# Kernel optimization log

Hardware: AMD Instinct MI355X
Metric: run time of the kernel (lower is better)

The kernel has to match this reference:

```python
import jax, jax.numpy as jnp
import numpy as np

N_NODES = 8192
N_EDGES = 524288
IN_DIM = 256
HID1 = 128
HID2 = 64


def setup_inputs() -> dict:
    key = jax.random.key(0)
    ks = jax.random.split(key, 10)
    s = 0.05
    x = jax.random.normal(ks[0], (N_NODES, IN_DIM), dtype=jnp.float32)
    edge_index = jax.random.randint(ks[1], (2, N_EDGES), 0, N_NODES, dtype=jnp.int64)
    W1 = jax.random.normal(ks[2], (IN_DIM, HID1), dtype=jnp.float32) * s
    b1 = jnp.zeros((HID1,), dtype=jnp.float32)
    W2 = jax.random.normal(ks[3], (IN_DIM, HID1), dtype=jnp.float32) * s
    b2 = jnp.zeros((HID1,), dtype=jnp.float32)
    Wmu = jax.random.normal(ks[4], (2 * HID1, HID2), dtype=jnp.float32) * s
    bmu = jnp.zeros((HID2,), dtype=jnp.float32)
    Wlv = jax.random.normal(ks[5], (2 * HID1, HID2), dtype=jnp.float32) * s
    blv = jnp.zeros((HID2,), dtype=jnp.float32)
    return {"x": x, "edge_index": edge_index, "W1": W1, "b1": b1,
            "W2": W2, "b2": b2, "Wmu": Wmu, "bmu": bmu, "Wlv": Wlv, "blv": blv}


def _gcn(x, W, b, row, col, norm, n):
    # linear transform, edge-indexed gather, degree-normalized scale, scatter-add
    h = x @ W                                   # [N, out]
    msg = h[col] * norm[:, None]                # [E+N, out]
    agg = jax.ops.segment_sum(msg, row, num_segments=n)
    return agg + b


def reference(x, edge_index, W1, b1, W2, b2, Wmu, bmu, Wlv, blv):
    n = x.shape[0]
    loop = jnp.arange(n, dtype=edge_index.dtype)
    row = jnp.concatenate([edge_index[0], loop])   # add self-loops (GCNConv default)
    col = jnp.concatenate([edge_index[1], loop])
    deg = jax.ops.segment_sum(jnp.ones_like(row, dtype=x.dtype), row, num_segments=n)
    dinv = jnp.where(deg > 0, jax.lax.rsqrt(deg), 0.0)
    norm = dinv[row] * dinv[col]                   # symmetric D^-1/2 A_hat D^-1/2

    h1 = _gcn(x, W1, b1, row, col, norm, n)
    h2 = _gcn(x, W2, b2, row, col, norm, n)
    hc = jnp.concatenate([h1, h2], axis=1)         # [N, 2*HID1]
    mu = _gcn(hc, Wmu, bmu, row, col, norm, n)
    logvar = _gcn(hc, Wlv, blv, row, col, norm, n)
    z = mu                                         # eval-mode reparametrize -> mu
    adj = jax.nn.sigmoid(z @ z.T)                  # InnerProductDecoder.forward_all
    return adj, mu, logvar
```

## Files before the change

kernel.cpp:

```cpp
#include <hip/hip_runtime.h>
#include <hip/hip_bf16.h>

#define N_NODES 8192
#define N_EDGES 524288
#define TOT_EDGES (N_EDGES + N_NODES)
#define IN_DIM 256
#define HID1 128
#define HID2 64
#define DC 128
#define CAP 192
#define FILL_BLK 520

typedef __attribute__((ext_vector_type(8))) short bf16x8;
typedef __attribute__((ext_vector_type(4))) float f32x4;
typedef __attribute__((ext_vector_type(4))) int   i32x4;
typedef __attribute__((ext_vector_type(4))) unsigned short u16x4;

__device__ __forceinline__ float b2f(unsigned short u){
    unsigned int v = ((unsigned int)u) << 16;
    float f; __builtin_memcpy(&f, &v, 4); return f;
}
__device__ __forceinline__ unsigned short f2b(float f){
    __hip_bfloat16 h = __float2bfloat16(f);
    return *(unsigned short*)&h;
}


__global__ __launch_bounds__(256) void k_pre(const float* __restrict__ W1, const float* __restrict__ W2,
                                             const float* __restrict__ Wmu, const float* __restrict__ Wlv,
                                             const float* __restrict__ b1, const float* __restrict__ b2,
                                             unsigned short* __restrict__ WcT, float* __restrict__ cvec,
                                             float* __restrict__ zbase){
    int b = blockIdx.x, t = threadIdx.x;
    if (b < 8){
        ((f32x4*)zbase)[b*256 + t] = (f32x4){0.f,0.f,0.f,0.f};
    } else {
        int r = (b - 8)*2 + (t >> 7);
        int j = t & 127;
        const float* Wsel = (j < 64) ? Wmu : Wlv;
        int jj = j & 63;
        float acc = 0.f;
        for (int k=0;k<HID1;k++){
            acc += W1[r*HID1+k] * Wsel[k*HID2+jj] + W2[r*HID1+k] * Wsel[(HID1+k)*HID2+jj];
        }
        WcT[(size_t)j*IN_DIM + r] = f2b(acc);
        if (r == 0){
            float c = 0.f;
            for (int k=0;k<HID1;k++){
                c += b1[k]*Wsel[k*HID2+jj] + b2[k]*Wsel[(HID1+k)*HID2+jj];
            }
            cvec[j] = c;
        }
    }
}


__global__ __launch_bounds__(256) void k_fill_gemm(const int* __restrict__ ei, int* __restrict__ fillc,
                                                   unsigned short* __restrict__ slots,
                                                   const float* __restrict__ x,
                                                   const unsigned short* __restrict__ WcT,
                                                   unsigned short* __restrict__ Ubf){
    int b = blockIdx.x, t = threadIdx.x;
    if (b < FILL_BLK){
        int e4 = (b*256 + t)*4;
        if (e4 >= TOT_EDGES) return;
        if (e4 < N_EDGES){
            i32x4 rr = *(const i32x4*)(ei + e4);
            i32x4 cc = *(const i32x4*)(ei + N_EDGES + e4);
            #pragma unroll
            for (int j=0;j<4;j++){
                int s = atomicAdd(&fillc[rr[j]], 1);
                if (s < CAP) slots[(size_t)rr[j]*CAP + s] = (unsigned short)cc[j];
            }
        } else {
            #pragma unroll
            for (int j=0;j<4;j++){
                int r = e4 - N_EDGES + j;
                int s = atomicAdd(&fillc[r], 1);
                if (s < CAP) slots[(size_t)r*CAP + s] = (unsigned short)r;
            }
        }
    } else {
        int l  = t & 63;
        int w  = t >> 6;
        int Ibase = (b - FILL_BLK)*32;
        int Jbase = w*32;
        int lr = l & 15;
        int kg = l >> 4;
        f32x4 acc[2][2];
        #pragma unroll
        for (int mt=0;mt<2;mt++)
            #pragma unroll
            for (int nt=0;nt<2;nt++) acc[mt][nt] = (f32x4){0.f,0.f,0.f,0.f};
        #pragma unroll
        for (int kc=0; kc<IN_DIM/32; kc++){
            bf16x8 a[2], bb[2];
            #pragma unroll
            for (int mt=0;mt<2;mt++){
                const float* xr = x + (size_t)(Ibase+mt*16+lr)*IN_DIM + kc*32 + kg*8;
                f32x4 v0 = *(const f32x4*)xr;
                f32x4 v1 = *(const f32x4*)(xr + 4);
                #pragma unroll
                for (int j=0;j<4;j++){
                    a[mt][j]   = (short)f2b(v0[j]);
                    a[mt][4+j] = (short)f2b(v1[j]);
                }
            }
            #pragma unroll
            for (int nt=0;nt<2;nt++)
                bb[nt] = *(const bf16x8*)(WcT + (size_t)(Jbase+nt*16+lr)*IN_DIM + kc*32 + kg*8);
            #pragma unroll
            for (int mt=0;mt<2;mt++)
                #pragma unroll
                for (int nt=0;nt<2;nt++)
                    acc[mt][nt] = __builtin_amdgcn_mfma_f32_16x16x32_bf16(a[mt], bb[nt], acc[mt][nt], 0, 0, 0);
        }
        #pragma unroll
        for (int mt=0;mt<2;mt++)
            #pragma unroll
            for (int r=0;r<4;r++){
                int grow = Ibase + mt*16 + kg*4 + r;
                #pragma unroll
                for (int nt=0;nt<2;nt++)
                    Ubf[(size_t)grow*DC + Jbase + nt*16 + lr] = f2b(acc[mt][nt][r]);
            }
    }
}


__global__ __launch_bounds__(256) void k_spmm(const unsigned short* __restrict__ IN,
                                              const unsigned short* __restrict__ slots,
                                              const int* __restrict__ fillc,
                                              unsigned short* __restrict__ OUT){
    int tid = threadIdx.x;
    int i = blockIdx.x*4 + (tid >> 6);
    int l  = tid & 15;
    int eg = (tid >> 4) & 3;
    int deg = min(fillc[i], CAP);
    const unsigned short* sl = slots + (size_t)i*CAP;
    float acc[8] = {0.f,0.f,0.f,0.f,0.f,0.f,0.f,0.f};
    for (int e = eg; e < deg; e += 4){
        int c = sl[e];
        float wgt = rsqrtf((float)fillc[c]);
        bf16x8 v = *(const bf16x8*)(IN + (size_t)c*DC + l*8);
        #pragma unroll
        for (int j=0;j<8;j++) acc[j] += wgt * b2f((unsigned short)v[j]);
    }
    #pragma unroll
    for (int j=0;j<8;j++){
        acc[j] += __shfl_xor(acc[j], 16);
        acc[j] += __shfl_xor(acc[j], 32);
    }
    if (eg == 0){
        float di = rsqrtf((float)fillc[i]);
        bf16x8 o;
        #pragma unroll
        for (int j=0;j<8;j++) o[j] = (short)f2b(di*acc[j]);
        *(bf16x8*)(OUT + (size_t)i*DC + l*8) = o;
    }
}


__global__ __launch_bounds__(256) void k_spmm_out(const unsigned short* __restrict__ T,
                                                  const unsigned short* __restrict__ slots,
                                                  const int* __restrict__ fillc,
                                                  const float* __restrict__ cvec,
                                                  const float* __restrict__ bmu, const float* __restrict__ blv,
                                                  float* __restrict__ outMu, float* __restrict__ outLv,
                                                  unsigned short* __restrict__ muBf){
    int tid = threadIdx.x;
    int i = blockIdx.x*4 + (tid >> 6);
    int l  = tid & 15;
    int eg = (tid >> 4) & 3;
    int deg = min(fillc[i], CAP);
    const unsigned short* sl = slots + (size_t)i*CAP;
    float acc[8] = {0.f,0.f,0.f,0.f,0.f,0.f,0.f,0.f};
    float wsum = 0.f;
    for (int e = eg; e < deg; e += 4){
        int c = sl[e];
        float wgt = rsqrtf((float)fillc[c]);
        wsum += wgt;
        bf16x8 v = *(const bf16x8*)(T + (size_t)c*DC + l*8);
        #pragma unroll
        for (int j=0;j<8;j++) acc[j] += wgt * b2f((unsigned short)v[j]);
    }
    #pragma unroll
    for (int j=0;j<8;j++){
        acc[j] += __shfl_xor(acc[j], 16);
        acc[j] += __shfl_xor(acc[j], 32);
    }
    wsum += __shfl_xor(wsum, 16);
    wsum += __shfl_xor(wsum, 32);
    if (eg == 0){
        float di = rsqrtf((float)fillc[i]);
        float sv = di * wsum;
        float val[8];
        #pragma unroll
        for (int j=0;j<8;j++) val[j] = di*acc[j] + sv*cvec[l*8+j];
        if (l < 8){
            f32x4 v0, v1; bf16x8 o;
            #pragma unroll
            for (int j=0;j<8;j++){
                float vv = val[j] + bmu[l*8+j];
                if (j<4) v0[j] = vv; else v1[j-4] = vv;
                o[j] = (short)f2b(vv);
            }
            *(f32x4*)(outMu + (size_t)i*HID2 + l*8)     = v0;
            *(f32x4*)(outMu + (size_t)i*HID2 + l*8 + 4) = v1;
            *(bf16x8*)(muBf + (size_t)i*HID2 + l*8)     = o;
        } else {
            int d = (l-8)*8;
            f32x4 v0, v1;
            #pragma unroll
            for (int j=0;j<8;j++){
                float vv = val[j] + blv[d+j];
                if (j<4) v0[j] = vv; else v1[j-4] = vv;
            }
            *(f32x4*)(outLv + (size_t)i*HID2 + d)     = v0;
            *(f32x4*)(outLv + (size_t)i*HID2 + d + 4) = v1;
        }
    }
}


__global__ __launch_bounds__(256) void k_adj(const unsigned short* __restrict__ mu, float* __restrict__ adj){
    int t  = threadIdx.x;
    int l  = t & 63;
    int w  = t >> 6;
    int wr = w >> 1, wc = w & 1;
    int Ibase = blockIdx.y*128 + wr*64;
    int Jbase = blockIdx.x*128 + wc*64;
    int lr = l & 15;
    int kg = l >> 4;

    bf16x8 afr[4][2], bfr[4][2];
    #pragma unroll
    for (int mt=0; mt<4; mt++){
        const unsigned short* p = mu + (size_t)(Ibase + mt*16 + lr)*HID2 + kg*8;
        afr[mt][0] = *(const bf16x8*)(p);
        afr[mt][1] = *(const bf16x8*)(p + 32);
    }
    #pragma unroll
    for (int nt=0; nt<4; nt++){
        const unsigned short* p = mu + (size_t)(Jbase + nt*16 + lr)*HID2 + kg*8;
        bfr[nt][0] = *(const bf16x8*)(p);
        bfr[nt][1] = *(const bf16x8*)(p + 32);
    }

    f32x4 acc[4][4];
    #pragma unroll
    for (int mt=0; mt<4; mt++)
        #pragma unroll
        for (int nt=0; nt<4; nt++)
            acc[mt][nt] = (f32x4){0.f,0.f,0.f,0.f};

    #pragma unroll
    for (int kc=0; kc<2; kc++)
        #pragma unroll
        for (int mt=0; mt<4; mt++)
            #pragma unroll
            for (int nt=0; nt<4; nt++)
                acc[mt][nt] = __builtin_amdgcn_mfma_f32_16x16x32_bf16(afr[mt][kc], bfr[nt][kc], acc[mt][nt], 0, 0, 0);

    __shared__ float wt[4][16][68];
    float* myt = &wt[w][0][0];
    #pragma unroll
    for (int mt=0; mt<4; mt++){
        asm volatile("s_waitcnt lgkmcnt(0)" ::: "memory");
        #pragma unroll
        for (int nt=0; nt<4; nt++)
            #pragma unroll
            for (int r=0; r<4; r++)
                myt[(kg*4+r)*68 + nt*16 + lr] = acc[mt][nt][r];
        asm volatile("s_waitcnt lgkmcnt(0)" ::: "memory");
        __builtin_amdgcn_sched_barrier(0);
        #pragma unroll
        for (int p=0; p<4; p++){
            int row = p*4 + (l >> 4);
            int col = (l & 15)*4;
            f32x4 v = *(const f32x4*)&myt[row*68 + col];
            f32x4 o;
            #pragma unroll
            for (int j=0;j<4;j++)
                o[j] = __builtin_amdgcn_rcpf(1.f + __expf(-v[j]));
            __builtin_nontemporal_store(o, (f32x4*)(adj + (size_t)(Ibase + mt*16 + row)*N_NODES + Jbase + col));
        }
    }
}


extern "C" void kernel_launch(void* const* d_in, const int* in_sizes, int n_in,
                              void* d_out, int out_size, void* d_ws, size_t ws_size,
                              hipStream_t stream){
    const float* x   = (const float*)d_in[0];
    const int*   ei  = (const int*)  d_in[1];
    const float* W1  = (const float*)d_in[2];
    const float* b1  = (const float*)d_in[3];
    const float* W2  = (const float*)d_in[4];
    const float* b2  = (const float*)d_in[5];
    const float* Wmu = (const float*)d_in[6];
    const float* bmu = (const float*)d_in[7];
    const float* Wlv = (const float*)d_in[8];
    const float* blv = (const float*)d_in[9];

    char* ws = (char*)d_ws;
    int*   fillc  = (int*)  (ws + 0);
    unsigned short* WcT = (unsigned short*)(ws + 32768);
    float* cvec   = (float*)(ws + 98304);
    unsigned short* muBf = (unsigned short*)(ws + 98816);

    float* adj   = (float*)d_out;
    float* outMu = adj + (size_t)N_NODES*N_NODES;
    float* outLv = outMu + (size_t)N_NODES*HID2;

    unsigned short* Ubf   = (unsigned short*)adj;
    unsigned short* Tbf   = (unsigned short*)((char*)adj + 16*1024*1024);
    unsigned short* slots = (unsigned short*)((char*)adj + 32*1024*1024);

    k_pre      <<<136, 256, 0, stream>>>(W1, W2, Wmu, Wlv, b1, b2, WcT, cvec, (float*)ws);
    k_fill_gemm<<<FILL_BLK + 256, 256, 0, stream>>>(ei, fillc, slots, x, WcT, Ubf);
    k_spmm     <<<N_NODES/4, 256, 0, stream>>>(Ubf, slots, fillc, Tbf);
    k_spmm_out <<<N_NODES/4, 256, 0, stream>>>(Tbf, slots, fillc, cvec, bmu, blv,
                                               outMu, outLv, muBf);
    k_adj      <<<dim3(N_NODES/128, N_NODES/128), 256, 0, stream>>>(muBf, adj);
}
```

Baseline: 126.8 us.

## Fold destination norm into first SpMM output so second SpMM skips per-edge weights

The first SpMM now adds the constant bias term and pre-scales each row by its own inverse-sqrt degree, so the second SpMM can sum neighbour rows without weights. This removes the per-edge fillc gather, rsqrt and weight-sum reduction from the second aggregation. The slot writes in the fill kernel become nontemporal stores, and both aggregation loops get unroll-2 hints. Storing the pre-scaled intermediate in bf16 changes rounding slightly.

Result: no change. 126.2 us (-0.4%).

```diff
diff --git a/kernel.cpp b/kernel.cpp
--- a/kernel.cpp
+++ b/kernel.cpp
@@ -70,14 +70,16 @@
             #pragma unroll
             for (int j=0;j<4;j++){
                 int s = atomicAdd(&fillc[rr[j]], 1);
-                if (s < CAP) slots[(size_t)rr[j]*CAP + s] = (unsigned short)cc[j];
+                if (s < CAP) __builtin_nontemporal_store((unsigned short)cc[j],
+                                 slots + (size_t)rr[j]*CAP + s);
             }
         } else {
             #pragma unroll
             for (int j=0;j<4;j++){
                 int r = e4 - N_EDGES + j;
                 int s = atomicAdd(&fillc[r], 1);
-                if (s < CAP) slots[(size_t)r*CAP + s] = (unsigned short)r;
+                if (s < CAP) __builtin_nontemporal_store((unsigned short)r,
+                                 slots + (size_t)r*CAP + s);
             }
         }
     } else {
@@ -131,6 +133,7 @@
 __global__ __launch_bounds__(256) void k_spmm(const unsigned short* __restrict__ IN,
                                               const unsigned short* __restrict__ slots,
                                               const int* __restrict__ fillc,
+                                              const float* __restrict__ cvec,
                                               unsigned short* __restrict__ OUT){
     int tid = threadIdx.x;
     int i = blockIdx.x*4 + (tid >> 6);
@@ -139,6 +142,7 @@
     int deg = min(fillc[i], CAP);
     const unsigned short* sl = slots + (size_t)i*CAP;
     float acc[8] = {0.f,0.f,0.f,0.f,0.f,0.f,0.f,0.f};
+    #pragma unroll 2
     for (int e = eg; e < deg; e += 4){
         int c = sl[e];
         float wgt = rsqrtf((float)fillc[c]);
@@ -155,7 +159,10 @@
         float di = rsqrtf((float)fillc[i]);
         bf16x8 o;
         #pragma unroll
-        for (int j=0;j<8;j++) o[j] = (short)f2b(di*acc[j]);
+        for (int j=0;j<8;j++){
+            float tprime = di*acc[j] + cvec[l*8+j];
+            o[j] = (short)f2b(di*tprime);
+        }
         *(bf16x8*)(OUT + (size_t)i*DC + l*8) = o;
     }
 }
@@ -164,7 +171,6 @@
 __global__ __launch_bounds__(256) void k_spmm_out(const unsigned short* __restrict__ T,
                                                   const unsigned short* __restrict__ slots,
                                                   const int* __restrict__ fillc,
-                                                  const float* __restrict__ cvec,
                                                   const float* __restrict__ bmu, const float* __restrict__ blv,
                                                   float* __restrict__ outMu, float* __restrict__ outLv,
                                                   unsigned short* __restrict__ muBf){
@@ -175,33 +181,25 @@
     int deg = min(fillc[i], CAP);
     const unsigned short* sl = slots + (size_t)i*CAP;
     float acc[8] = {0.f,0.f,0.f,0.f,0.f,0.f,0.f,0.f};
-    float wsum = 0.f;
+    #pragma unroll 2
     for (int e = eg; e < deg; e += 4){
         int c = sl[e];
-        float wgt = rsqrtf((float)fillc[c]);
-        wsum += wgt;
         bf16x8 v = *(const bf16x8*)(T + (size_t)c*DC + l*8);
         #pragma unroll
-        for (int j=0;j<8;j++) acc[j] += wgt * b2f((unsigned short)v[j]);
+        for (int j=0;j<8;j++) acc[j] += b2f((unsigned short)v[j]);
     }
     #pragma unroll
     for (int j=0;j<8;j++){
         acc[j] += __shfl_xor(acc[j], 16);
         acc[j] += __shfl_xor(acc[j], 32);
     }
-    wsum += __shfl_xor(wsum, 16);
-    wsum += __shfl_xor(wsum, 32);
     if (eg == 0){
         float di = rsqrtf((float)fillc[i]);
-        float sv = di * wsum;
-        float val[8];
-        #pragma unroll
-        for (int j=0;j<8;j++) val[j] = di*acc[j] + sv*cvec[l*8+j];
         if (l < 8){
             f32x4 v0, v1; bf16x8 o;
             #pragma unroll
             for (int j=0;j<8;j++){
-                float vv = val[j] + bmu[l*8+j];
+                float vv = di*acc[j] + bmu[l*8+j];
                 if (j<4) v0[j] = vv; else v1[j-4] = vv;
                 o[j] = (short)f2b(vv);
             }
@@ -213,7 +211,7 @@
             f32x4 v0, v1;
             #pragma unroll
             for (int j=0;j<8;j++){
-                float vv = val[j] + blv[d+j];
+                float vv = di*acc[j] + blv[d+j];
                 if (j<4) v0[j] = vv; else v1[j-4] = vv;
             }
             *(f32x4*)(outLv + (size_t)i*HID2 + d)     = v0;
@@ -319,8 +317,8 @@
 
     k_pre      <<<136, 256, 0, stream>>>(W1, W2, Wmu, Wlv, b1, b2, WcT, cvec, (float*)ws);
     k_fill_gemm<<<FILL_BLK + 256, 256, 0, stream>>>(ei, fillc, slots, x, WcT, Ubf);
-    k_spmm     <<<N_NODES/4, 256, 0, stream>>>(Ubf, slots, fillc, Tbf);
-    k_spmm_out <<<N_NODES/4, 256, 0, stream>>>(Tbf, slots, fillc, cvec, bmu, blv,
+    k_spmm     <<<N_NODES/4, 256, 0, stream>>>(Ubf, slots, fillc, cvec, Tbf);
+    k_spmm_out <<<N_NODES/4, 256, 0, stream>>>(Tbf, slots, fillc, bmu, blv,
                                                outMu, outLv, muBf);
     k_adj      <<<dim3(N_NODES/128, N_NODES/128), 256, 0, stream>>>(muBf, adj);
 }
```
